# Optimization experiments

Measured on AMD Instinct MI355X. Metric: run time of the kernel, lower is better.

## Reference

```python
import jax, jax.numpy as jnp
import numpy as np

N_BINS = 15


def setup_inputs() -> dict:
    key = jax.random.key(0)
    k1, k2 = jax.random.split(key)
    N, C = 1000000, 100
    logits = jax.random.normal(k1, (N, C), dtype=jnp.float32)
    labels = jax.random.randint(k2, (N,), 0, C, dtype=jnp.int64)
    return {"logits": logits, "labels": labels}


def reference(logits, labels):
    # softmax probs, top-1 confidence and prediction
    probs = jax.nn.softmax(logits, axis=1)
    confidences = jnp.max(probs, axis=1)            # [N]
    predictions = jnp.argmax(probs, axis=1)         # [N]
    accuracies = (predictions == labels).astype(jnp.float32)

    n = confidences.shape[0]
    # bin b covers (b/n_bins, (b+1)/n_bins]; conf>0 always since softmax max >= 1/C
    bin_idx = jnp.clip(
        jnp.ceil(confidences * N_BINS).astype(jnp.int32) - 1, 0, N_BINS - 1
    )
    counts = jax.ops.segment_sum(
        jnp.ones_like(confidences), bin_idx, num_segments=N_BINS
    )
    conf_sums = jax.ops.segment_sum(confidences, bin_idx, num_segments=N_BINS)
    acc_sums = jax.ops.segment_sum(accuracies, bin_idx, num_segments=N_BINS)

    prop_in_bin = counts / n
    denom = jnp.maximum(counts, 1.0)
    avg_conf = conf_sums / denom
    avg_acc = acc_sums / denom
    per_bin = jnp.where(
        counts > 0, jnp.abs(avg_conf - avg_acc) * prop_in_bin, 0.0
    )
    ece = jnp.sum(per_bin)
    return ece.reshape(1)
```

## Files before the change

### kernel.cpp

```cpp
#include <hip/hip_runtime.h>

#define NBINS 15
#define ROWS 128
#define BLK 128
#define NC 100
#define SEGS 50
#define NSLOT 32
#define SSTR 48

typedef __attribute__((address_space(3))) unsigned int lds_u32_t;
typedef const __attribute__((address_space(1))) unsigned int glob_u32_t;

__global__ __launch_bounds__(BLK) void ece_main(
    const float* __restrict__ logits,
    const int* __restrict__ labels,
    float* __restrict__ ws, int N) {
  __shared__ float smem[ROWS * NC];
  __shared__ float s_hist[3 * NBINS];

  const int tid = threadIdx.x;
  const int lane = tid & 63;
  const int wv = tid >> 6;
  if (tid < 3 * NBINS) s_hist[tid] = 0.f;

  const size_t total_bytes = (size_t)N * NC * 4;
  const size_t chunk_byte = (size_t)blockIdx.x * (ROWS * NC * 4);
  #pragma unroll
  for (int k = 0; k < SEGS / 2; ++k) {
    const int seg = 2 * k + wv;
    const size_t gb = chunk_byte + (size_t)seg * 1024;
    if (gb < total_bytes) {
      const char* g = (const char*)logits + gb + (size_t)lane * 16;
      float* l = smem + seg * 256;
      __builtin_amdgcn_global_load_lds((glob_u32_t*)g, (lds_u32_t*)l, 16, 0, 0);
    }
  }
  asm volatile("s_waitcnt vmcnt(0)" ::: "memory");
  __syncthreads();

  const int row = blockIdx.x * ROWS + tid;
  if (row < N) {
    const float4* r4 = (const float4*)(smem + tid * NC);

    float4 bv = r4[0];
    int bix = 0, biy = 1, biz = 2, biw = 3;
    #pragma unroll
    for (int j = 1; j < NC / 4; ++j) {
      float4 u = r4[j];
      if (u.x > bv.x) { bv.x = u.x; bix = 4 * j; }
      if (u.y > bv.y) { bv.y = u.y; biy = 4 * j + 1; }
      if (u.z > bv.z) { bv.z = u.z; biz = 4 * j + 2; }
      if (u.w > bv.w) { bv.w = u.w; biw = 4 * j + 3; }
    }
    float m = bv.x; int mi = bix;
    if (bv.y > m || (bv.y == m && biy < mi)) { m = bv.y; mi = biy; }
    if (bv.z > m || (bv.z == m && biz < mi)) { m = bv.z; mi = biz; }
    if (bv.w > m || (bv.w == m && biw < mi)) { m = bv.w; mi = biw; }

    float sx = 0.f, sy = 0.f, sz = 0.f, sw = 0.f;
    #pragma unroll
    for (int j = 0; j < NC / 4; ++j) {
      float4 u = r4[j];
      sx += __expf(u.x - m);
      sy += __expf(u.y - m);
      sz += __expf(u.z - m);
      sw += __expf(u.w - m);
    }
    float conf = 1.0f / ((sx + sy) + (sz + sw));

    int b = (int)ceilf(conf * (float)NBINS) - 1;
    b = b < 0 ? 0 : (b > NBINS - 1 ? NBINS - 1 : b);
    float acc = (mi == labels[row]) ? 1.0f : 0.0f;
    atomicAdd(&s_hist[b], 1.0f);
    atomicAdd(&s_hist[NBINS + b], conf);
    atomicAdd(&s_hist[2 * NBINS + b], acc);
  }
  __syncthreads();

  if (tid < 3 * NBINS) {
    float v = s_hist[tid];
    if (v != 0.f)
      atomicAdd(&ws[(blockIdx.x & (NSLOT - 1)) * SSTR + tid], v);
  }
}

__global__ void ece_final(const float* __restrict__ ws,
                          float* __restrict__ out, int N) {
  __shared__ float per_bin[NBINS];
  const int b = threadIdx.x;
  if (b < NBINS) {
    float cnt = 0.f, cf = 0.f, ac = 0.f;
    #pragma unroll
    for (int s = 0; s < NSLOT; ++s) {
      cnt += ws[s * SSTR + b];
      cf  += ws[s * SSTR + NBINS + b];
      ac  += ws[s * SSTR + 2 * NBINS + b];
    }
    float d = fmaxf(cnt, 1.0f);
    per_bin[b] = (cnt > 0.f) ? fabsf(cf / d - ac / d) * (cnt / (float)N) : 0.f;
  }
  __syncthreads();
  if (b == 0) {
    float e = 0.f;
    #pragma unroll
    for (int i = 0; i < NBINS; ++i) e += per_bin[i];
    out[0] = e;
  }
}

extern "C" void kernel_launch(void* const* d_in, const int* in_sizes, int n_in,
                              void* d_out, int out_size, void* d_ws, size_t ws_size,
                              hipStream_t stream) {
  const float* logits = (const float*)d_in[0];
  const int* labels = (const int*)d_in[1];
  const int N = in_sizes[1];
  float* ws = (float*)d_ws;
  float* out = (float*)d_out;

  hipMemsetAsync(ws, 0, NSLOT * SSTR * sizeof(float), stream);
  const int grid = (N + ROWS - 1) / ROWS;
  ece_main<<<grid, BLK, 0, stream>>>(logits, labels, ws, N);
  ece_final<<<1, 64, 0, stream>>>(ws, out, N);
}
```

Baseline: 90.74 us.

## Use persistent single-wave blocks with double-buffered LDS staging of logits and labels

Replaces the one-block-per-128-rows grid with a fixed grid of 768 single-wave blocks. Each block loops over 64-row chunks and double-buffers them in LDS, issuing the async global-to-LDS loads for the next chunk before computing the current one. Labels are now staged through LDS too, and any leftover tail rows are handled by block 0 reading straight from global memory. The aim is to overlap HBM traffic with the softmax and argmax work and to cut block launch and reduction overhead. The cost is fewer waves per CU, which may reduce latency hiding, and a fixed grid size.

```diff
diff --git a/kernel.cpp b/kernel.cpp
--- a/kernel.cpp
+++ b/kernel.cpp
@@ -1,86 +1,110 @@
 #include <hip/hip_runtime.h>
 
 #define NBINS 15
-#define ROWS 128
-#define BLK 128
-#define NC 100
-#define SEGS 50
+#define RPC   64
+#define SEGS  25
+#define BUF_FLTS (RPC * 100 + RPC)
 #define NSLOT 32
-#define SSTR 48
+#define SSTR  48
+#define GRID  768
 
 typedef __attribute__((address_space(3))) unsigned int lds_u32_t;
 typedef const __attribute__((address_space(1))) unsigned int glob_u32_t;
 
-__global__ __launch_bounds__(BLK) void ece_main(
-    const float* __restrict__ logits,
-    const int* __restrict__ labels,
+__device__ __forceinline__ void stage_chunk(const float* __restrict__ logits,
+                                            const int* __restrict__ labels,
+                                            long long chunk, float* lbase, int lane) {
+  const char* gbase = (const char*)logits + chunk * (long long)(RPC * 100 * 4);
+  #pragma unroll
+  for (int seg = 0; seg < SEGS; ++seg) {
+    const char* g = gbase + seg * 1024 + lane * 16;
+    __builtin_amdgcn_global_load_lds((glob_u32_t*)g, (lds_u32_t*)(lbase + seg * 256),
+                                     16, 0, 0);
+  }
+  const char* gl = (const char*)(labels + chunk * RPC + lane);
+  __builtin_amdgcn_global_load_lds((glob_u32_t*)gl, (lds_u32_t*)(lbase + RPC * 100),
+                                   4, 0, 0);
+}
+
+__device__ __forceinline__ void row_reduce(const float4* __restrict__ r4,
+                                           float& conf, int& mi) {
+  float4 bv = r4[0];
+  int bix = 0, biy = 1, biz = 2, biw = 3;
+  #pragma unroll
+  for (int j = 1; j < 25; ++j) {
+    float4 u = r4[j];
+    if (u.x > bv.x) { bv.x = u.x; bix = 4 * j; }
+    if (u.y > bv.y) { bv.y = u.y; biy = 4 * j + 1; }
+    if (u.z > bv.z) { bv.z = u.z; biz = 4 * j + 2; }
+    if (u.w > bv.w) { bv.w = u.w; biw = 4 * j + 3; }
+  }
+  float m = bv.x; mi = bix;
+  if (bv.y > m || (bv.y == m && biy < mi)) { m = bv.y; mi = biy; }
+  if (bv.z > m || (bv.z == m && biz < mi)) { m = bv.z; mi = biz; }
+  if (bv.w > m || (bv.w == m && biw < mi)) { m = bv.w; mi = biw; }
+
+  float sx = 0.f, sy = 0.f, sz = 0.f, sw = 0.f;
+  #pragma unroll
+  for (int j = 0; j < 25; ++j) {
+    float4 u = r4[j];
+    sx += __expf(u.x - m);
+    sy += __expf(u.y - m);
+    sz += __expf(u.z - m);
+    sw += __expf(u.w - m);
+  }
+  conf = 1.0f / ((sx + sy) + (sz + sw));
+}
+
+__device__ __forceinline__ void bin_and_add(float conf, int mi, int lab,
+                                            float* s_hist) {
+  int b = (int)ceilf(conf * (float)NBINS) - 1;
+  b = b < 0 ? 0 : (b > NBINS - 1 ? NBINS - 1 : b);
+  atomicAdd(&s_hist[b], 1.0f);
+  atomicAdd(&s_hist[NBINS + b], conf);
+  atomicAdd(&s_hist[2 * NBINS + b], (mi == lab) ? 1.0f : 0.0f);
+}
+
+__global__ __launch_bounds__(64) void ece_main(
+    const float* __restrict__ logits, const int* __restrict__ labels,
     float* __restrict__ ws, int N) {
-  __shared__ float smem[ROWS * NC];
+  __shared__ float smem[2 * BUF_FLTS];
   __shared__ float s_hist[3 * NBINS];
+  const int lane = threadIdx.x;
+  if (lane < 3 * NBINS) s_hist[lane] = 0.f;
 
-  const int tid = threadIdx.x;
-  const int lane = tid & 63;
-  const int wv = tid >> 6;
-  if (tid < 3 * NBINS) s_hist[tid] = 0.f;
+  const long long nfull = (long long)N / RPC;
+  long long c = blockIdx.x;
+  int cur = 0;
+  if (c < nfull) stage_chunk(logits, labels, c, smem, lane);
 
-  const size_t total_bytes = (size_t)N * NC * 4;
-  const size_t chunk_byte = (size_t)blockIdx.x * (ROWS * NC * 4);
-  #pragma unroll
-  for (int k = 0; k < SEGS / 2; ++k) {
-    const int seg = 2 * k + wv;
-    const size_t gb = chunk_byte + (size_t)seg * 1024;
-    if (gb < total_bytes) {
-      const char* g = (const char*)logits + gb + (size_t)lane * 16;
-      float* l = smem + seg * 256;
-      __builtin_amdgcn_global_load_lds((glob_u32_t*)g, (lds_u32_t*)l, 16, 0, 0);
+  for (; c < nfull; c += gridDim.x) {
+    const long long nx = c + gridDim.x;
+    if (nx < nfull) {
+      stage_chunk(logits, labels, nx, smem + (cur ^ 1) * BUF_FLTS, lane);
+      asm volatile("s_waitcnt vmcnt(26)" ::: "memory");
+    } else {
+      asm volatile("s_waitcnt vmcnt(0)" ::: "memory");
     }
+    const float* lbase = smem + cur * BUF_FLTS;
+    float conf; int mi;
+    row_reduce((const float4*)(lbase + lane * 100), conf, mi);
+    const int lab = ((const int*)(lbase + RPC * 100))[lane];
+    bin_and_add(conf, mi, lab, s_hist);
+    cur ^= 1;
   }
-  asm volatile("s_waitcnt vmcnt(0)" ::: "memory");
+
+  const long long trow = nfull * RPC + lane;
+  if (blockIdx.x == 0 && trow < N) {
+    float conf; int mi;
+    row_reduce((const float4*)(logits + trow * 100), conf, mi);
+    bin_and_add(conf, mi, labels[trow], s_hist);
+  }
+
   __syncthreads();
-
-  const int row = blockIdx.x * ROWS + tid;
-  if (row < N) {
-    const float4* r4 = (const float4*)(smem + tid * NC);
-
-    float4 bv = r4[0];
-    int bix = 0, biy = 1, biz = 2, biw = 3;
-    #pragma unroll
-    for (int j = 1; j < NC / 4; ++j) {
-      float4 u = r4[j];
-      if (u.x > bv.x) { bv.x = u.x; bix = 4 * j; }
-      if (u.y > bv.y) { bv.y = u.y; biy = 4 * j + 1; }
-      if (u.z > bv.z) { bv.z = u.z; biz = 4 * j + 2; }
-      if (u.w > bv.w) { bv.w = u.w; biw = 4 * j + 3; }
-    }
-    float m = bv.x; int mi = bix;
-    if (bv.y > m || (bv.y == m && biy < mi)) { m = bv.y; mi = biy; }
-    if (bv.z > m || (bv.z == m && biz < mi)) { m = bv.z; mi = biz; }
-    if (bv.w > m || (bv.w == m && biw < mi)) { m = bv.w; mi = biw; }
-
-    float sx = 0.f, sy = 0.f, sz = 0.f, sw = 0.f;
-    #pragma unroll
-    for (int j = 0; j < NC / 4; ++j) {
-      float4 u = r4[j];
-      sx += __expf(u.x - m);
-      sy += __expf(u.y - m);
-      sz += __expf(u.z - m);
-      sw += __expf(u.w - m);
-    }
-    float conf = 1.0f / ((sx + sy) + (sz + sw));
-
-    int b = (int)ceilf(conf * (float)NBINS) - 1;
-    b = b < 0 ? 0 : (b > NBINS - 1 ? NBINS - 1 : b);
-    float acc = (mi == labels[row]) ? 1.0f : 0.0f;
-    atomicAdd(&s_hist[b], 1.0f);
-    atomicAdd(&s_hist[NBINS + b], conf);
-    atomicAdd(&s_hist[2 * NBINS + b], acc);
-  }
-  __syncthreads();
-
-  if (tid < 3 * NBINS) {
-    float v = s_hist[tid];
+  if (lane < 3 * NBINS) {
+    float v = s_hist[lane];
     if (v != 0.f)
-      atomicAdd(&ws[(blockIdx.x & (NSLOT - 1)) * SSTR + tid], v);
+      atomicAdd(&ws[(blockIdx.x & (NSLOT - 1)) * SSTR + lane], v);
   }
 }
 
@@ -118,7 +142,6 @@
   float* out = (float*)d_out;
 
   hipMemsetAsync(ws, 0, NSLOT * SSTR * sizeof(float), stream);
-  const int grid = (N + ROWS - 1) / ROWS;
-  ece_main<<<grid, BLK, 0, stream>>>(logits, labels, ws, N);
+  ece_main<<<GRID, 64, 0, stream>>>(logits, labels, ws, N);
   ece_final<<<1, 64, 0, stream>>>(ws, out, N);
 }
```

Result: faster. 88.43 us (-2.5%).

## Load logits directly into registers with four threads per row

Applied to the files above, without the earlier changes.

Drops the LDS staging via global_load_lds and instead has four threads cooperate on each row, each loading float4 chunks straight into registers. Argmax and the softmax sum are reduced across the four lanes with xor shuffles, and only lane 0 updates the shared histogram. Blocks grow to 256 threads covering 64 rows, and the global slot count grows to 256 to spread the atomics. The per-thread loads are strided by 64 bytes inside a row, so coalescing depends on neighbouring lanes filling in the gaps, and the final kernel now has to sum more slots.

```diff
diff --git a/kernel.cpp b/kernel.cpp
--- a/kernel.cpp
+++ b/kernel.cpp
@@ -1,79 +1,73 @@
 #include <hip/hip_runtime.h>
 
 #define NBINS 15
-#define ROWS 128
-#define BLK 128
-#define NC 100
-#define SEGS 50
-#define NSLOT 32
-#define SSTR 48
+#define NSLOT 256
+#define SSTR  48
+#define NC    100
 
-typedef __attribute__((address_space(3))) unsigned int lds_u32_t;
-typedef const __attribute__((address_space(1))) unsigned int glob_u32_t;
-
-__global__ __launch_bounds__(BLK) void ece_main(
+__global__ __launch_bounds__(256) void ece_main(
     const float* __restrict__ logits,
     const int* __restrict__ labels,
     float* __restrict__ ws, int N) {
-  __shared__ float smem[ROWS * NC];
   __shared__ float s_hist[3 * NBINS];
-
   const int tid = threadIdx.x;
-  const int lane = tid & 63;
-  const int wv = tid >> 6;
   if (tid < 3 * NBINS) s_hist[tid] = 0.f;
-
-  const size_t total_bytes = (size_t)N * NC * 4;
-  const size_t chunk_byte = (size_t)blockIdx.x * (ROWS * NC * 4);
-  #pragma unroll
-  for (int k = 0; k < SEGS / 2; ++k) {
-    const int seg = 2 * k + wv;
-    const size_t gb = chunk_byte + (size_t)seg * 1024;
-    if (gb < total_bytes) {
-      const char* g = (const char*)logits + gb + (size_t)lane * 16;
-      float* l = smem + seg * 256;
-      __builtin_amdgcn_global_load_lds((glob_u32_t*)g, (lds_u32_t*)l, 16, 0, 0);
-    }
-  }
-  asm volatile("s_waitcnt vmcnt(0)" ::: "memory");
   __syncthreads();
 
-  const int row = blockIdx.x * ROWS + tid;
+  const int q = tid & 3;
+  const int row = blockIdx.x * 64 + (tid >> 2);
   if (row < N) {
-    const float4* r4 = (const float4*)(smem + tid * NC);
+    const float4* rp4 = (const float4*)(logits + (long long)row * NC);
 
-    float4 bv = r4[0];
-    int bix = 0, biy = 1, biz = 2, biw = 3;
+    float4 f[7];
     #pragma unroll
-    for (int j = 1; j < NC / 4; ++j) {
-      float4 u = r4[j];
-      if (u.x > bv.x) { bv.x = u.x; bix = 4 * j; }
-      if (u.y > bv.y) { bv.y = u.y; biy = 4 * j + 1; }
-      if (u.z > bv.z) { bv.z = u.z; biz = 4 * j + 2; }
-      if (u.w > bv.w) { bv.w = u.w; biw = 4 * j + 3; }
+    for (int j = 0; j < 6; ++j) f[j] = rp4[q + 4 * j];
+    f[6] = make_float4(-INFINITY, -INFINITY, -INFINITY, -INFINITY);
+    if (q == 0) f[6] = rp4[24];
+
+    float bx = f[0].x, by = f[0].y, bz = f[0].z, bw = f[0].w;
+    int kx = q, ky = q, kz = q, kw = q;
+    #pragma unroll
+    for (int j = 1; j < 7; ++j) {
+      const int k = (j < 6) ? (q + 4 * j) : 24;
+      if (f[j].x > bx) { bx = f[j].x; kx = k; }
+      if (f[j].y > by) { by = f[j].y; ky = k; }
+      if (f[j].z > bz) { bz = f[j].z; kz = k; }
+      if (f[j].w > bw) { bw = f[j].w; kw = k; }
     }
-    float m = bv.x; int mi = bix;
-    if (bv.y > m || (bv.y == m && biy < mi)) { m = bv.y; mi = biy; }
-    if (bv.z > m || (bv.z == m && biz < mi)) { m = bv.z; mi = biz; }
-    if (bv.w > m || (bv.w == m && biw < mi)) { m = bv.w; mi = biw; }
+    float m = bx; int mi = 4 * kx;
+    if (by > m || (by == m && 4 * ky + 1 < mi)) { m = by; mi = 4 * ky + 1; }
+    if (bz > m || (bz == m && 4 * kz + 2 < mi)) { m = bz; mi = 4 * kz + 2; }
+    if (bw > m || (bw == m && 4 * kw + 3 < mi)) { m = bw; mi = 4 * kw + 3; }
+
+    #pragma unroll
+    for (int off = 1; off <= 2; off <<= 1) {
+      float ov = __shfl_xor(m, off);
+      int   oi = __shfl_xor(mi, off);
+      if (ov > m || (ov == m && oi < mi)) { m = ov; mi = oi; }
+    }
 
     float sx = 0.f, sy = 0.f, sz = 0.f, sw = 0.f;
     #pragma unroll
-    for (int j = 0; j < NC / 4; ++j) {
-      float4 u = r4[j];
-      sx += __expf(u.x - m);
-      sy += __expf(u.y - m);
-      sz += __expf(u.z - m);
-      sw += __expf(u.w - m);
+    for (int j = 0; j < 7; ++j) {
+      sx += __expf(f[j].x - m);
+      sy += __expf(f[j].y - m);
+      sz += __expf(f[j].z - m);
+      sw += __expf(f[j].w - m);
     }
-    float conf = 1.0f / ((sx + sy) + (sz + sw));
+    float s = (sx + sy) + (sz + sw);
+    #pragma unroll
+    for (int off = 1; off <= 2; off <<= 1) s += __shfl_xor(s, off);
 
-    int b = (int)ceilf(conf * (float)NBINS) - 1;
-    b = b < 0 ? 0 : (b > NBINS - 1 ? NBINS - 1 : b);
-    float acc = (mi == labels[row]) ? 1.0f : 0.0f;
-    atomicAdd(&s_hist[b], 1.0f);
-    atomicAdd(&s_hist[NBINS + b], conf);
-    atomicAdd(&s_hist[2 * NBINS + b], acc);
+    if (q == 0) {
+      float conf = 1.0f / s;
+      int b = (int)ceilf(conf * (float)NBINS) - 1;
+      b = b < 0 ? 0 : (b > NBINS - 1 ? NBINS - 1 : b);
+      float acc = (mi == labels[row]) ? 1.0f : 0.0f;
+      atomicAdd(&s_hist[b], 1.0f);
+      atomicAdd(&s_hist[NBINS + b], conf);
+      atomicAdd(&s_hist[2 * NBINS + b], acc);
+    }
   }
   __syncthreads();
 
@@ -90,7 +84,7 @@
   const int b = threadIdx.x;
   if (b < NBINS) {
     float cnt = 0.f, cf = 0.f, ac = 0.f;
-    #pragma unroll
+    #pragma unroll 8
     for (int s = 0; s < NSLOT; ++s) {
       cnt += ws[s * SSTR + b];
       cf  += ws[s * SSTR + NBINS + b];
@@ -118,7 +112,7 @@
   float* out = (float*)d_out;
 
   hipMemsetAsync(ws, 0, NSLOT * SSTR * sizeof(float), stream);
-  const int grid = (N + ROWS - 1) / ROWS;
-  ece_main<<<grid, BLK, 0, stream>>>(logits, labels, ws, N);
+  const int grid = (N + 63) / 64;
+  ece_main<<<grid, 256, 0, stream>>>(logits, labels, ws, N);
   ece_final<<<1, 64, 0, stream>>>(ws, out, N);
 }
```

After: 88.79 us. -2.1%, faster.
